# Kernel optimization log

Hardware: AMD Instinct MI355X
Metric: run time of the kernel (lower is better)

The kernel has to match this reference:

```python
import jax, jax.numpy as jnp
import numpy as np

NUM_EMB = 8192
EMB_DIM = 64
TOP_K = 10
TEMP = 1.0
PERP_W = 0.01


def setup_inputs() -> dict:
    key = jax.random.key(0)
    k1, k2, k3 = jax.random.split(key, 3)
    inputs = jax.random.normal(k1, (8, 2048, EMB_DIM), dtype=jnp.float32)
    codebook = jax.random.normal(k2, (NUM_EMB, EMB_DIM), dtype=jnp.float32)
    # Gumbel noise for vectorized multinomial sampling over top-k (Gumbel-max trick)
    u = jax.random.uniform(k3, (8 * 2048, TOP_K), dtype=jnp.float32, minval=1e-6, maxval=1.0 - 1e-6)
    gumbel = -jnp.log(-jnp.log(u))
    return {"inputs": inputs, "codebook": codebook, "gumbel": gumbel}


def _vq_forward(inputs, codebook, gumbel):
    K, D = codebook.shape
    shp = inputs.shape
    flat = inputs.reshape(-1, D)                      # [N, D]
    valid = jnp.linalg.norm(flat, axis=1) > 1e-6      # [N]
    d = (jnp.sum(flat * flat, axis=1, keepdims=True)
         + jnp.sum(codebook * codebook, axis=1)
         - 2.0 * (flat @ codebook.T))
    # top-k smallest distances
    neg_top, top_idx = jax.lax.top_k(-d, TOP_K)       # [N, k]
    top_d = -neg_top
    logits = -top_d / TEMP
    # multinomial(softmax(logits)) sample per row via Gumbel-max (vectorized)
    j = jnp.argmax(logits + gumbel, axis=1)           # [N]
    rows = jnp.arange(flat.shape[0])
    idx = top_idx[rows, j]                            # sampled codebook indices [N]
    min_d = top_d[rows, j]                            # sampled distances [N]
    q_valid = codebook[idx]                           # embedding gather [N, D]
    vmask = valid[:, None].astype(flat.dtype)
    q_flat = q_valid * vmask                          # zero rows where invalid
    idx_flat = jnp.where(valid, idx, 0)
    min_d_flat = jnp.where(valid, min_d, jnp.zeros((), flat.dtype))
    n_valid = jnp.maximum(jnp.sum(valid.astype(flat.dtype)), 1.0)
    # codebook (VQ) loss: MSE over valid rows; commitment loss has 0 weight in source
    loss_vq = jnp.sum(vmask * (q_valid - jax.lax.stop_gradient(flat)) ** 2) / (n_valid * D)
    quantized = q_flat.reshape(shp)
    quantized_st = inputs + jax.lax.stop_gradient(quantized - inputs)
    # usage / perplexity from one-hot scatter-add over valid rows
    counts = jnp.zeros(K, dtype=flat.dtype).at[idx].add(valid.astype(flat.dtype))
    avg_probs = counts / n_valid
    perplexity = jnp.exp(-jnp.sum(avg_probs * jnp.log(avg_probs + 1e-10)))
    perplexity_loss = -jnp.log(perplexity + 1e-10)
    total_loss = loss_vq + PERP_W * perplexity_loss
    return quantized_st, total_loss, idx_flat, min_d_flat, perplexity


def reference(inputs, codebook, gumbel):
    return _vq_forward(inputs, codebook, gumbel)
```

## Files before the change

### kernel.cpp

```cpp
#include <hip/hip_runtime.h>
#include <hip/hip_bf16.h>

#define N_ROWS   16384
#define EMB_DIM  64
#define NUM_EMB  8192
#define TOP_K    10
#define PERP_W   0.01

#define M_CHUNK   12

#define QST_OFF   0
#define LOSS_OFF  (N_ROWS * EMB_DIM)
#define IDX_OFF   (LOSS_OFF + 1)
#define MIND_OFF  (IDX_OFF + N_ROWS)
#define PERP_OFF  (MIND_OFF + N_ROWS)

#define WS_E2C    0
#define WS_E2D    32768
#define WS_CBS    98304
#define WS_HIST   1146880
#define WS_LOSSP  1179648
#define WS_NVP    1212416
#define WS_C32    1228800

typedef short bf16x8 __attribute__((ext_vector_type(8)));
typedef float f32x4  __attribute__((ext_vector_type(4)));

__device__ __forceinline__ unsigned umx(unsigned a, unsigned b) {
    return __builtin_elementwise_max(a, b);
}
__device__ __forceinline__ unsigned umn(unsigned a, unsigned b) {
    return __builtin_elementwise_min(a, b);
}

__device__ __forceinline__ unsigned short f2bf(float f) {
    unsigned int u = __float_as_uint(f);
    unsigned int r = u + 0x7fffu + ((u >> 16) & 1u);
    return (unsigned short)(r >> 16);
}

__global__ __launch_bounds__(256) void vq_prep(const float* __restrict__ cb,
                                               float* __restrict__ e2c,
                                               double* __restrict__ e2d,
                                               unsigned short* __restrict__ cbs,
                                               int* __restrict__ hist) {
    const int g  = blockIdx.x * 256 + threadIdx.x;
    const int k  = g >> 2;
    const int lq = g & 3;

    if (g < NUM_EMB) hist[g] = 0;

    const float4* rp = (const float4*)(cb + (size_t)k * EMB_DIM + lq * 16);
    float  s  = 0.0f;
    double sd = 0.0;
    unsigned pk[8];
#pragma unroll
    for (int i = 0; i < 4; ++i) {
        const float4 v = rp[i];
        s  += v.x * v.x + v.y * v.y + v.z * v.z + v.w * v.w;
        sd += (double)v.x * (double)v.x + (double)v.y * (double)v.y
            + (double)v.z * (double)v.z + (double)v.w * (double)v.w;
        pk[2 * i + 0] = (unsigned)f2bf(v.x) | ((unsigned)f2bf(v.y) << 16);
        pk[2 * i + 1] = (unsigned)f2bf(v.z) | ((unsigned)f2bf(v.w) << 16);
    }
    s  += __shfl_xor(s, 1);  s  += __shfl_xor(s, 2);
    sd += __shfl_xor(sd, 1); sd += __shfl_xor(sd, 2);
    if (lq == 0) { e2c[k] = 512.0f - 0.5f * s; e2d[k] = sd; }

    const int tp = k >> 5, r32 = k & 31, rsub = r32 & 15;
    unsigned short* basep = cbs + ((size_t)tp << 11)
                          + ((unsigned)(r32 & 16) << 6)
                          + (rsub << 3);
    const int hi  = lq >> 1;
    const int q2s = (lq & 1) * 2;
    uint4 c0, c1;
    c0.x = pk[0]; c0.y = pk[1]; c0.z = pk[2]; c0.w = pk[3];
    c1.x = pk[4]; c1.y = pk[5]; c1.z = pk[6]; c1.w = pk[7];
    *(uint4*)(basep + hi * 512 + (q2s + 0) * 128) = c0;
    *(uint4*)(basep + hi * 512 + (q2s + 1) * 128) = c1;
}

__global__ __launch_bounds__(256) void vq_gemm_topk(
        const float* __restrict__ inp, const unsigned short* __restrict__ cbs,
        const float* __restrict__ e2c, unsigned short* __restrict__ cand32) {
    __shared__ unsigned keysh[16][193];

    const int tid   = threadIdx.x;
    const int w     = tid >> 6;
    const int lane  = tid & 63;
    const int q     = lane >> 4;
    const int rsub  = lane & 15;
    const int row0  = blockIdx.x * 16;
    const int row   = row0 + rsub;
    const int half0 = blockIdx.y * 4096;
    const int cbase = half0 + w * 1024;
    const int tpbase = cbase >> 5;

    const int eoff = q << 2;

    bf16x8 b0, b1;
    {
        const float* xp = inp + (size_t)row * EMB_DIM + q * 8;
#pragma unroll
        for (int j = 0; j < 8; ++j) b0[j] = (short)f2bf(xp[j]);
#pragma unroll
        for (int j = 0; j < 8; ++j) b1[j] = (short)f2bf(xp[32 + j]);
    }

    unsigned la[12], lb[12];
#pragma unroll
    for (int i = 0; i < 12; ++i) { la[i] = 0u; lb[i] = 0u; }

#define LOADP(P0,P1,P2,P3,E0,E1,TT) { \
        const bf16x8* bp_ = ((const bf16x8*)cbs) + (size_t)(tpbase + (TT)) * 256; \
        P0 = bp_[lane];        P1 = bp_[lane + 64]; \
        P2 = bp_[lane + 128];  P3 = bp_[lane + 192]; \
        const float* ep_ = e2c + cbase + (TT) * 32; \
        E0 = *(const f32x4*)(ep_ + eoff); \
        E1 = *(const f32x4*)(ep_ + eoff + 16); }

    bf16x8 A00, A01, A10, A11, B00, B01, B10, B11;
    f32x4  Ae0, Ae1, Be0, Be1;
    LOADP(A00, A01, A10, A11, Ae0, Ae1, 0)
    LOADP(B00, B01, B10, B11, Be0, Be1, 1)

#define CE(A,B) { const unsigned mx_ = umx(A, B), mn_ = umn(A, B); \
                  A = mx_; B = mn_; }

#define SORT3(A,B,C) { const unsigned x3_ = A, y3_ = B, z3_ = C; \
        unsigned mx3_, md3_, mn3_; \
        asm("v_max3_u32 %0, %1, %2, %3" : "=v"(mx3_) : "v"(x3_), "v"(y3_), "v"(z3_)); \
        asm("v_med3_u32 %0, %1, %2, %3" : "=v"(md3_) : "v"(x3_), "v"(y3_), "v"(z3_)); \
        asm("v_min3_u32 %0, %1, %2, %3" : "=v"(mn3_) : "v"(x3_), "v"(y3_), "v"(z3_)); \
        A = mx3_; B = md3_; C = mn3_; }

#define RESORT(L) { \
        CE(L[0],L[6]) CE(L[1],L[7]) CE(L[2],L[8])  CE(L[3],L[9])  CE(L[4],L[10]) CE(L[5],L[11]) \
        CE(L[0],L[3]) CE(L[1],L[4]) CE(L[2],L[5])  CE(L[6],L[9])  CE(L[7],L[10]) CE(L[8],L[11]) \
        SORT3(L[0],L[1],L[2]) SORT3(L[3],L[4],L[5]) \
        SORT3(L[6],L[7],L[8]) SORT3(L[9],L[10],L[11]) }

#define SUBITER(P0,P1,P2,P3,E0,E1,TT,TP,L) { \
        const bf16x8 c00_ = P0, c01_ = P1, c10_ = P2, c11_ = P3; \
        const f32x4  ce0_ = E0, ce1_ = E1; \
        LOADP(P0, P1, P2, P3, E0, E1, (TP) & 31) \
        f32x4 acc0_ = __builtin_amdgcn_mfma_f32_16x16x32_bf16(c00_, b0, ce0_, 0, 0, 0); \
        acc0_       = __builtin_amdgcn_mfma_f32_16x16x32_bf16(c01_, b1, acc0_, 0, 0, 0); \
        f32x4 acc1_ = __builtin_amdgcn_mfma_f32_16x16x32_bf16(c10_, b0, ce1_, 0, 0, 0); \
        acc1_       = __builtin_amdgcn_mfma_f32_16x16x32_bf16(c11_, b1, acc1_, 0, 0, 0); \
        const unsigned tb_ = (unsigned)((TT) << 3); \
        unsigned k0 = (__float_as_uint(acc0_[0]) & 0xFFFFFF00u) | (tb_ + 0u); \
        unsigned k1 = (__float_as_uint(acc0_[1]) & 0xFFFFFF00u) | (tb_ + 1u); \
        unsigned k2 = (__float_as_uint(acc0_[2]) & 0xFFFFFF00u) | (tb_ + 2u); \
        unsigned k3 = (__float_as_uint(acc0_[3]) & 0xFFFFFF00u) | (tb_ + 3u); \
        unsigned k4 = (__float_as_uint(acc1_[0]) & 0xFFFFFF00u) | (tb_ + 4u); \
        unsigned k5 = (__float_as_uint(acc1_[1]) & 0xFFFFFF00u) | (tb_ + 5u); \
        unsigned k6 = (__float_as_uint(acc1_[2]) & 0xFFFFFF00u) | (tb_ + 6u); \
        unsigned k7 = (__float_as_uint(acc1_[3]) & 0xFFFFFF00u) | (tb_ + 7u); \
         \
        CE(k0,k1) CE(k2,k3) CE(k4,k5) CE(k6,k7) \
        CE(k0,k2) CE(k1,k3) CE(k4,k6) CE(k5,k7) \
        CE(k1,k2) CE(k5,k6) \
        CE(k0,k4) CE(k1,k5) CE(k2,k6) CE(k3,k7) \
        CE(k2,k4) CE(k3,k5) \
        CE(k1,k2) CE(k3,k4) CE(k5,k6) \
         \
         \
        CE(L[11],k0) CE(L[10],k1) CE(L[9],k2) CE(L[8],k3) \
        CE(L[7],k4)  CE(L[6],k5)  CE(L[5],k6) CE(L[4],k7) \
        RESORT(L) }

    for (int t = 0; t < 32; t += 2) {
        SUBITER(A00, A01, A10, A11, Ae0, Ae1, t,     t + 2, la)
        SUBITER(B00, B01, B10, B11, Be0, Be1, t + 1, t + 3, lb)
    }
#undef SUBITER
#undef LOADP

    CE(la[11], lb[0]) CE(la[10], lb[1]) CE(la[9], lb[2])  CE(la[8], lb[3])
    CE(la[7],  lb[4]) CE(la[6],  lb[5]) CE(la[5], lb[6])  CE(la[4], lb[7])
    CE(la[3],  lb[8]) CE(la[2],  lb[9]) CE(la[1], lb[10]) CE(la[0], lb[11])
    RESORT(la)
#undef RESORT
#undef SORT3
#undef CE

    {
        unsigned* kr = &keysh[rsub][w * 48 + q * 12];
#pragma unroll
        for (int i = 0; i < 12; ++i) kr[i] = la[i];
    }
    __syncthreads();

    for (int rr = 0; rr < 4; ++rr) {
        const int lr = 4 * w + rr;
        const unsigned ka = keysh[lr][lane];
        const unsigned kb = keysh[lr][lane + 64];
        const unsigned kc = keysh[lr][lane + 128];

        unsigned tau = 0u;
#pragma unroll
        for (int b = 31; b >= 0; --b) {
            const unsigned t2 = tau | (1u << b);
            const int cnt = __popcll(__ballot(ka >= t2))
                          + __popcll(__ballot(kb >= t2))
                          + __popcll(__ballot(kc >= t2));
            if (cnt >= 16) tau = t2;
        }

        const unsigned long long m0 = __ballot(ka >= tau);
        const unsigned long long m1 = __ballot(kb >= tau);
        const unsigned long long m2 = __ballot(kc >= tau);
        const unsigned long long below = (lane == 0) ? 0ull
                                        : (~0ull >> (64 - lane));
        const int c0 = __popcll(m0);
        const int c1 = __popcll(m1);
        const int p0 = __popcll(m0 & below);
        const int p1 = c0 + __popcll(m1 & below);
        const int p2 = c0 + c1 + __popcll(m2 & below);

        unsigned short* outp =
            cand32 + (size_t)(row0 + lr) * 32 + blockIdx.y * 16;

#define EMIT(KX, SLOT, POS) \
        if ((KX) >= tau && (POS) < 16) { \
            const unsigned slot_ = (unsigned)(SLOT); \
            const unsigned idx_  = (KX) & 0xFFu; \
            const unsigned wq_   = slot_ / 48u; \
            const unsigned qq_   = (slot_ % 48u) / 12u; \
            const unsigned code_ = (unsigned)half0 + wq_ * 1024u \
                                 + ((idx_ >> 3) << 5) + (((idx_ >> 2) & 1u) << 4) \
                                 + (qq_ << 2) + (idx_ & 3u); \
            outp[POS] = (unsigned short)code_; \
        }
        EMIT(ka, lane,       p0)
        EMIT(kb, lane + 64,  p1)
        EMIT(kc, lane + 128, p2)
#undef EMIT
    }
}

__global__ __launch_bounds__(256) void vq_finalize(const float* __restrict__ inp,
                                                   const float* __restrict__ cb,
                                                   const double* __restrict__ e2d,
                                                   const float* __restrict__ gumbel,
                                                   const unsigned short* __restrict__ cand32,
                                                   float* __restrict__ out,
                                                   int* __restrict__ hist,
                                                   double* __restrict__ lossp,
                                                   int* __restrict__ nvp) {
    __shared__ double dvs[4][32];
    __shared__ int    dis[4][32];
    __shared__ double wl[4];
    __shared__ int    wv[4];

    const int tid  = threadIdx.x;
    const int w    = tid >> 6;
    const int lane = tid & 63;
    const int row  = blockIdx.x * 4 + w;
    const int g    = lane >> 2;
    const int lq   = lane & 3;

    const float xf = inp[(size_t)row * EMB_DIM + lane];
    const double xd = (double)xf;

    const int code0 = (int)cand32[(size_t)row * 32 + g];
    const int code1 = (int)cand32[(size_t)row * 32 + 16 + g];
    const float4* ep0 = (const float4*)(cb + ((size_t)code0 << 6) + (lq << 4));
    const float4* ep1 = (const float4*)(cb + ((size_t)code1 << 6) + (lq << 4));
    const float4 a0 = ep0[0], a1 = ep0[1], a2 = ep0[2], a3 = ep0[3];
    const float4 b0 = ep1[0], b1 = ep1[1], b2 = ep1[2], b3 = ep1[3];
    const double ed0 = e2d[code0];
    const double ed1 = e2d[code1];

    double x2 = xd * xd;
#pragma unroll
    for (int off = 32; off >= 1; off >>= 1) x2 += __shfl_xor(x2, off);
    const bool valid = sqrt(x2) > 1e-6;

    double xq[16];
    {
        const float4* xp = (const float4*)(inp + (size_t)row * EMB_DIM + (lq << 4));
#pragma unroll
        for (int i = 0; i < 4; ++i) {
            const float4 v = xp[i];
            xq[4 * i + 0] = (double)v.x; xq[4 * i + 1] = (double)v.y;
            xq[4 * i + 2] = (double)v.z; xq[4 * i + 3] = (double)v.w;
        }
    }

#define DOT16(V0,V1,V2,V3, EDV, J, CODE) { \
        double d0_ = 0.0, d1_ = 0.0; \
        d0_ = fma(xq[0],  (double)V0.x, d0_);  d0_ = fma(xq[1],  (double)V0.y, d0_); \
        d0_ = fma(xq[2],  (double)V0.z, d0_);  d0_ = fma(xq[3],  (double)V0.w, d0_); \
        d0_ = fma(xq[4],  (double)V1.x, d0_);  d0_ = fma(xq[5],  (double)V1.y, d0_); \
        d0_ = fma(xq[6],  (double)V1.z, d0_);  d0_ = fma(xq[7],  (double)V1.w, d0_); \
        d1_ = fma(xq[8],  (double)V2.x, d1_);  d1_ = fma(xq[9],  (double)V2.y, d1_); \
        d1_ = fma(xq[10], (double)V2.z, d1_);  d1_ = fma(xq[11], (double)V2.w, d1_); \
        d1_ = fma(xq[12], (double)V3.x, d1_);  d1_ = fma(xq[13], (double)V3.y, d1_); \
        d1_ = fma(xq[14], (double)V3.z, d1_);  d1_ = fma(xq[15], (double)V3.w, d1_); \
        double dot_ = d0_ + d1_; \
        dot_ += __shfl_xor(dot_, 1); \
        dot_ += __shfl_xor(dot_, 2); \
        if (lq == 0) { \
            dvs[w][J] = x2 + (EDV) - 2.0 * dot_; \
            dis[w][J] = (CODE); \
        } }

    DOT16(a0, a1, a2, a3, ed0, g,      code0)
    DOT16(b0, b1, b2, b3, ed1, 16 + g, code1)
#undef DOT16
    __syncthreads();

    const bool has = (lane < 32);
    double cd = has ? dvs[w][lane] : 1.0e300;
    int    ci = has ? dis[w][lane] : 0x7fffffff;

    int rank = 0;
#pragma unroll
    for (int off = 1; off < 32; ++off) {
        const double od = __shfl_xor(cd, off);
        const int    oi = __shfl_xor(ci, off);
        if (od < cd || (od == cd && oi < ci)) ++rank;
    }

    float sc = -3.0e38f;
    if (has && rank < TOP_K)
        sc = (float)(-cd) + gumbel[(size_t)row * TOP_K + rank];

    double bd = cd; int bi = ci; int brk = rank;
#pragma unroll
    for (int off = 1; off < 64; off <<= 1) {
        const float  os = __shfl_xor(sc, off);
        const double od = __shfl_xor(bd, off);
        const int    oi = __shfl_xor(bi, off);
        const int    ork = __shfl_xor(brk, off);
        if (os > sc || (os == sc && ork < brk)) {
            sc = os; bd = od; bi = oi; brk = ork;
        }
    }
    const int   cidx = bi;
    const float mind = (float)bd;

    const float vm = valid ? 1.0f : 0.0f;
    const float qv = cb[(size_t)cidx * EMB_DIM + lane];
    out[QST_OFF + (size_t)row * EMB_DIM + lane] = xf + (qv * vm - xf);

    const double dq = (double)qv - xd;
    double l = dq * dq * (double)vm;
#pragma unroll
    for (int off = 32; off >= 1; off >>= 1) l += __shfl_xor(l, off);

    if (lane == 0) {
        wl[w] = l;
        wv[w] = valid ? 1 : 0;
        if (valid) atomicAdd(&hist[cidx], 1);
        out[IDX_OFF + row]  = valid ? (float)cidx : 0.0f;
        out[MIND_OFF + row] = valid ? mind : 0.0f;
    }
    __syncthreads();
    if (tid == 0) {
        lossp[blockIdx.x] = wl[0] + wl[1] + wl[2] + wl[3];
        nvp[blockIdx.x]   = wv[0] + wv[1] + wv[2] + wv[3];
    }
}

__global__ __launch_bounds__(1024) void vq_scalars(const double* __restrict__ lossp,
                                                   const int* __restrict__ nvp,
                                                   const int* __restrict__ hist,
                                                   float* __restrict__ out) {
    __shared__ double red[1024];
    __shared__ double s_nv;
    const int tid = threadIdx.x;

    double lsum = 0.0;
    int    nvl  = 0;
#pragma unroll
    for (int i = 0; i < 4; ++i) {
        const int j = tid + 1024 * i;
        lsum += lossp[j];
        nvl  += nvp[j];
    }

    red[tid] = lsum;
    __syncthreads();
    for (int s = 512; s >= 1; s >>= 1) {
        if (tid < s) red[tid] += red[tid + s];
        __syncthreads();
    }
    const double losstot = red[0];
    __syncthreads();

    red[tid] = (double)nvl;
    __syncthreads();
    for (int s = 512; s >= 1; s >>= 1) {
        if (tid < s) red[tid] += red[tid + s];
        __syncthreads();
    }
    if (tid == 0) s_nv = (red[0] > 0.5) ? red[0] : 1.0;
    __syncthreads();
    const double nv = s_nv;
    __syncthreads();

    double h = 0.0;
#pragma unroll
    for (int i = 0; i < 8; ++i) {
        const int k = tid + 1024 * i;
        const double p = (double)hist[k] / nv;
        h += p * log(p + 1e-10);
    }
    red[tid] = h;
    __syncthreads();
    for (int s = 512; s >= 1; s >>= 1) {
        if (tid < s) red[tid] += red[tid + s];
        __syncthreads();
    }
    if (tid == 0) {
        const double H = red[0];
        const double perp = exp(-H);
        const double ploss = -log(perp + 1e-10);
        const double lvq = losstot / (nv * (double)EMB_DIM);
        out[LOSS_OFF] = (float)(lvq + PERP_W * ploss);
        out[PERP_OFF] = (float)perp;
    }
}

extern "C" void kernel_launch(void* const* d_in, const int* in_sizes, int n_in,
                              void* d_out, int out_size, void* d_ws, size_t ws_size,
                              hipStream_t stream) {
    const float* inp    = (const float*)d_in[0];
    const float* cb     = (const float*)d_in[1];
    const float* gumbel = (const float*)d_in[2];
    float* out = (float*)d_out;

    char* ws = (char*)d_ws;
    float*          e2c    = (float*)(ws + WS_E2C);
    double*         e2d    = (double*)(ws + WS_E2D);
    unsigned short* cbs    = (unsigned short*)(ws + WS_CBS);
    int*            hist   = (int*)(ws + WS_HIST);
    double*         lossp  = (double*)(ws + WS_LOSSP);
    int*            nvp    = (int*)(ws + WS_NVP);
    unsigned short* cand32 = (unsigned short*)(ws + WS_C32);

    vq_prep<<<NUM_EMB * 4 / 256, 256, 0, stream>>>(cb, e2c, e2d, cbs, hist);
    vq_gemm_topk<<<dim3(N_ROWS / 16, 2), 256, 0, stream>>>(inp, cbs, e2c, cand32);
    vq_finalize<<<N_ROWS / 4, 256, 0, stream>>>(inp, cb, e2d, gumbel, cand32, out,
                                                hist, lossp, nvp);
    vq_scalars<<<1, 1024, 0, stream>>>(lossp, nvp, hist, out);
}
```

Baseline: 178.8 us.

## Process 32 rows per block to reuse codebook tiles across two row groups

The GEMM+top-k kernel now handles two 16-row groups per block. Each loaded codebook tile feeds MFMAs for both groups, which halves global codebook traffic per row. The two running top-12 lists, previously used as interleaved halves for one row group, now each track a separate row group, so the final merge is dropped. The grid halves and register pressure rises (four B fragments, more accumulators), which may cut occupancy and leave fewer blocks to fill the device.

```diff
diff --git a/kernel.cpp b/kernel.cpp
--- a/kernel.cpp
+++ b/kernel.cpp
@@ -7,7 +7,6 @@
 #define TOP_K    10
 #define PERP_W   0.01
 
-#define M_CHUNK   12
 
 #define QST_OFF   0
 #define LOSS_OFF  (N_ROWS * EMB_DIM)
@@ -83,28 +82,34 @@
 __global__ __launch_bounds__(256) void vq_gemm_topk(
         const float* __restrict__ inp, const unsigned short* __restrict__ cbs,
         const float* __restrict__ e2c, unsigned short* __restrict__ cand32) {
-    __shared__ unsigned keysh[16][193];
+    __shared__ unsigned keysh[32][193];
 
     const int tid   = threadIdx.x;
     const int w     = tid >> 6;
     const int lane  = tid & 63;
     const int q     = lane >> 4;
     const int rsub  = lane & 15;
-    const int row0  = blockIdx.x * 16;
-    const int row   = row0 + rsub;
+    const int row0  = blockIdx.x * 32;
+    const int rowA  = row0 + rsub;
+    const int rowB  = row0 + 16 + rsub;
     const int half0 = blockIdx.y * 4096;
     const int cbase = half0 + w * 1024;
     const int tpbase = cbase >> 5;
 
     const int eoff = q << 2;
 
-    bf16x8 b0, b1;
+    bf16x8 b0, b1, b2, b3;
     {
-        const float* xp = inp + (size_t)row * EMB_DIM + q * 8;
-#pragma unroll
-        for (int j = 0; j < 8; ++j) b0[j] = (short)f2bf(xp[j]);
-#pragma unroll
-        for (int j = 0; j < 8; ++j) b1[j] = (short)f2bf(xp[32 + j]);
+        const float* xpA = inp + (size_t)rowA * EMB_DIM + q * 8;
+        const float* xpB = inp + (size_t)rowB * EMB_DIM + q * 8;
+#pragma unroll
+        for (int j = 0; j < 8; ++j) b0[j] = (short)f2bf(xpA[j]);
+#pragma unroll
+        for (int j = 0; j < 8; ++j) b1[j] = (short)f2bf(xpA[32 + j]);
+#pragma unroll
+        for (int j = 0; j < 8; ++j) b2[j] = (short)f2bf(xpB[j]);
+#pragma unroll
+        for (int j = 0; j < 8; ++j) b3[j] = (short)f2bf(xpB[32 + j]);
     }
 
     unsigned la[12], lb[12];
@@ -140,7 +145,20 @@
         SORT3(L[0],L[1],L[2]) SORT3(L[3],L[4],L[5]) \
         SORT3(L[6],L[7],L[8]) SORT3(L[9],L[10],L[11]) }
 
-#define SUBITER(P0,P1,P2,P3,E0,E1,TT,TP,L) { \
+#define SORT8(k0,k1,k2,k3,k4,k5,k6,k7) \
+        CE(k0,k1) CE(k2,k3) CE(k4,k5) CE(k6,k7) \
+        CE(k0,k2) CE(k1,k3) CE(k4,k6) CE(k5,k7) \
+        CE(k1,k2) CE(k5,k6) \
+        CE(k0,k4) CE(k1,k5) CE(k2,k6) CE(k3,k7) \
+        CE(k2,k4) CE(k3,k5) \
+        CE(k1,k2) CE(k3,k4) CE(k5,k6)
+
+#define MERGE12(L,k0,k1,k2,k3,k4,k5,k6,k7) \
+        CE(L[11],k0) CE(L[10],k1) CE(L[9],k2) CE(L[8],k3) \
+        CE(L[7],k4)  CE(L[6],k5)  CE(L[5],k6) CE(L[4],k7) \
+        RESORT(L)
+
+#define SUBITER(P0,P1,P2,P3,E0,E1,TT,TP) { \
         const bf16x8 c00_ = P0, c01_ = P1, c10_ = P2, c11_ = P3; \
         const f32x4  ce0_ = E0, ce1_ = E1; \
         LOADP(P0, P1, P2, P3, E0, E1, (TP) & 31) \
@@ -148,6 +166,10 @@
         acc0_       = __builtin_amdgcn_mfma_f32_16x16x32_bf16(c01_, b1, acc0_, 0, 0, 0); \
         f32x4 acc1_ = __builtin_amdgcn_mfma_f32_16x16x32_bf16(c10_, b0, ce1_, 0, 0, 0); \
         acc1_       = __builtin_amdgcn_mfma_f32_16x16x32_bf16(c11_, b1, acc1_, 0, 0, 0); \
+        f32x4 acc2_ = __builtin_amdgcn_mfma_f32_16x16x32_bf16(c00_, b2, ce0_, 0, 0, 0); \
+        acc2_       = __builtin_amdgcn_mfma_f32_16x16x32_bf16(c01_, b3, acc2_, 0, 0, 0); \
+        f32x4 acc3_ = __builtin_amdgcn_mfma_f32_16x16x32_bf16(c10_, b2, ce1_, 0, 0, 0); \
+        acc3_       = __builtin_amdgcn_mfma_f32_16x16x32_bf16(c11_, b3, acc3_, 0, 0, 0); \
         const unsigned tb_ = (unsigned)((TT) << 3); \
         unsigned k0 = (__float_as_uint(acc0_[0]) & 0xFFFFFF00u) | (tb_ + 0u); \
         unsigned k1 = (__float_as_uint(acc0_[1]) & 0xFFFFFF00u) | (tb_ + 1u); \
@@ -157,43 +179,43 @@
         unsigned k5 = (__float_as_uint(acc1_[1]) & 0xFFFFFF00u) | (tb_ + 5u); \
         unsigned k6 = (__float_as_uint(acc1_[2]) & 0xFFFFFF00u) | (tb_ + 6u); \
         unsigned k7 = (__float_as_uint(acc1_[3]) & 0xFFFFFF00u) | (tb_ + 7u); \
-         \
-        CE(k0,k1) CE(k2,k3) CE(k4,k5) CE(k6,k7) \
-        CE(k0,k2) CE(k1,k3) CE(k4,k6) CE(k5,k7) \
-        CE(k1,k2) CE(k5,k6) \
-        CE(k0,k4) CE(k1,k5) CE(k2,k6) CE(k3,k7) \
-        CE(k2,k4) CE(k3,k5) \
-        CE(k1,k2) CE(k3,k4) CE(k5,k6) \
-         \
-         \
-        CE(L[11],k0) CE(L[10],k1) CE(L[9],k2) CE(L[8],k3) \
-        CE(L[7],k4)  CE(L[6],k5)  CE(L[5],k6) CE(L[4],k7) \
-        RESORT(L) }
+        unsigned m0 = (__float_as_uint(acc2_[0]) & 0xFFFFFF00u) | (tb_ + 0u); \
+        unsigned m1 = (__float_as_uint(acc2_[1]) & 0xFFFFFF00u) | (tb_ + 1u); \
+        unsigned m2 = (__float_as_uint(acc2_[2]) & 0xFFFFFF00u) | (tb_ + 2u); \
+        unsigned m3 = (__float_as_uint(acc2_[3]) & 0xFFFFFF00u) | (tb_ + 3u); \
+        unsigned m4 = (__float_as_uint(acc3_[0]) & 0xFFFFFF00u) | (tb_ + 4u); \
+        unsigned m5 = (__float_as_uint(acc3_[1]) & 0xFFFFFF00u) | (tb_ + 5u); \
+        unsigned m6 = (__float_as_uint(acc3_[2]) & 0xFFFFFF00u) | (tb_ + 6u); \
+        unsigned m7 = (__float_as_uint(acc3_[3]) & 0xFFFFFF00u) | (tb_ + 7u); \
+        SORT8(k0,k1,k2,k3,k4,k5,k6,k7) \
+        SORT8(m0,m1,m2,m3,m4,m5,m6,m7) \
+        MERGE12(la, k0,k1,k2,k3,k4,k5,k6,k7) \
+        MERGE12(lb, m0,m1,m2,m3,m4,m5,m6,m7) }
 
     for (int t = 0; t < 32; t += 2) {
-        SUBITER(A00, A01, A10, A11, Ae0, Ae1, t,     t + 2, la)
-        SUBITER(B00, B01, B10, B11, Be0, Be1, t + 1, t + 3, lb)
+        SUBITER(A00, A01, A10, A11, Ae0, Ae1, t,     t + 2)
+        SUBITER(B00, B01, B10, B11, Be0, Be1, t + 1, t + 3)
     }
 #undef SUBITER
-#undef LOADP
-
-    CE(la[11], lb[0]) CE(la[10], lb[1]) CE(la[9], lb[2])  CE(la[8], lb[3])
-    CE(la[7],  lb[4]) CE(la[6],  lb[5]) CE(la[5], lb[6])  CE(la[4], lb[7])
-    CE(la[3],  lb[8]) CE(la[2],  lb[9]) CE(la[1], lb[10]) CE(la[0], lb[11])
-    RESORT(la)
+#undef MERGE12
+#undef SORT8
 #undef RESORT
 #undef SORT3
 #undef CE
+#undef LOADP
 
     {
-        unsigned* kr = &keysh[rsub][w * 48 + q * 12];
-#pragma unroll
-        for (int i = 0; i < 12; ++i) kr[i] = la[i];
-    }
-    __syncthreads();
-
-    for (int rr = 0; rr < 4; ++rr) {
-        const int lr = 4 * w + rr;
+        unsigned* kr0 = &keysh[rsub][w * 48 + q * 12];
+        unsigned* kr1 = &keysh[rsub + 16][w * 48 + q * 12];
+#pragma unroll
+        for (int i = 0; i < 12; ++i) kr0[i] = la[i];
+#pragma unroll
+        for (int i = 0; i < 12; ++i) kr1[i] = lb[i];
+    }
+    __syncthreads();
+
+    for (int rr = 0; rr < 8; ++rr) {
+        const int lr = 8 * w + rr;
         const unsigned ka = keysh[lr][lane];
         const unsigned kb = keysh[lr][lane + 64];
         const unsigned kc = keysh[lr][lane + 128];
@@ -443,7 +465,7 @@
     unsigned short* cand32 = (unsigned short*)(ws + WS_C32);
 
     vq_prep<<<NUM_EMB * 4 / 256, 256, 0, stream>>>(cb, e2c, e2d, cbs, hist);
-    vq_gemm_topk<<<dim3(N_ROWS / 16, 2), 256, 0, stream>>>(inp, cbs, e2c, cand32);
+    vq_gemm_topk<<<dim3(N_ROWS / 32, 2), 256, 0, stream>>>(inp, cbs, e2c, cand32);
     vq_finalize<<<N_ROWS / 4, 256, 0, stream>>>(inp, cb, e2d, gumbel, cand32, out,
                                                 hist, lossp, nvp);
     vq_scalars<<<1, 1024, 0, stream>>>(lossp, nvp, hist, out);
```

Measured after the change: 182.9 us. 1.02x slower.
